# Optimization experiments

Hardware: AMD Instinct MI355X
Metric: run time of the kernel (lower is better)

## Reference

```python
import jax, jax.numpy as jnp
import numpy as np

EMBED_DIM = 1024
NUM_HEADS = 16
HEAD_DIM = EMBED_DIM // NUM_HEADS
SCALE = HEAD_DIM ** -0.5


def setup_inputs() -> dict:
    key = jax.random.key(0)
    ks = jax.random.split(key, 11)
    b, n, c = 2, 2048, EMBED_DIM
    # xavier_uniform bound for square [c, c] weight
    bound = float(np.sqrt(6.0 / (c + c)))
    def xavier(k):
        return jax.random.uniform(k, (c, c), jnp.float32, -bound, bound)
    return {
        "q": jax.random.normal(ks[0], (b, n, c), jnp.float32),
        "k": jax.random.normal(ks[1], (b, n, c), jnp.float32),
        "v": jax.random.normal(ks[2], (b, n, c), jnp.float32),
        "wq": xavier(ks[3]), "bq": jnp.zeros((c,), jnp.float32),
        "wk": xavier(ks[4]), "bk": jnp.zeros((c,), jnp.float32),
        "wv": xavier(ks[5]), "bv": jnp.zeros((c,), jnp.float32),
        "wo": xavier(ks[6]), "bo": jnp.zeros((c,), jnp.float32),
    }


def reference(q, k, v, wq, bq, wk, bk, wv, bv, wo, bo):
    b, n, c = q.shape
    h, d = NUM_HEADS, HEAD_DIM
    # linear projections (torch Linear: x @ W^T + b)
    qh = (q @ wq.T + bq).reshape(b, n, h, d).transpose(0, 2, 1, 3)  # b h n d
    kh = (k @ wk.T + bk).reshape(b, n, h, d).transpose(0, 2, 1, 3)
    vh = (v @ wv.T + bv).reshape(b, n, h, d).transpose(0, 2, 1, 3)
    dots = jnp.einsum('bhid,bhjd->bhij', qh, kh) * SCALE
    attn = jax.nn.softmax(dots, axis=-1)  # dropout p=0 -> identity
    out = jnp.einsum('bhij,bhjd->bhid', attn, vh)
    out = out.transpose(0, 2, 1, 3).reshape(b, n, c)
    return out @ wo.T + bo
```

## Files before the change

### kernel.cpp

```cpp
#include <hip/hip_runtime.h>


typedef float f32x4 __attribute__((ext_vector_type(4)));
typedef float f32x16 __attribute__((ext_vector_type(16)));
typedef __bf16 bf16x8 __attribute__((ext_vector_type(8)));

#define SEQ 2048
#define CH 1024
#define NH 16
#define HD 64
#define TOK 4096
#define QSCALE 0.18033688011112042f

__device__ __forceinline__ unsigned short f2b(float f) {
  unsigned int u = __float_as_uint(f);
  u = (u + 0x7FFFu + ((u >> 16) & 1u)) >> 16;
  return (unsigned short)u;
}

__device__ __forceinline__ unsigned int cvtpk(float lo, float hi) {
  unsigned int r;
  asm("v_cvt_pk_bf16_f32 %0, %1, %2" : "=v"(r) : "v"(lo), "v"(hi));
  return r;
}

__device__ __forceinline__ void gload16(const void* g, void* l) {
  __builtin_amdgcn_global_load_lds(
      (const __attribute__((address_space(1))) unsigned int*)g,
      (__attribute__((address_space(3))) unsigned int*)l, 16, 0, 0);
}

struct CvtArgs {
  const float* src[7];
  unsigned short* dst[7];
  int n4[7];
};

__global__ __launch_bounds__(256) void cvt_kernel(CvtArgs a) {
  const int s = blockIdx.y;
  const int n4 = a.n4[s];
  const float4* __restrict__ src = (const float4*)a.src[s];
  unsigned short* __restrict__ dst = a.dst[s];
  const int stride = gridDim.x * blockDim.x;
  for (int i = blockIdx.x * blockDim.x + threadIdx.x; i < n4; i += stride) {
    float4 w = src[i];
    ushort4 o;
    o.x = f2b(w.x); o.y = f2b(w.y); o.z = f2b(w.z); o.w = f2b(w.w);
    *(ushort4*)(dst + 4 * (size_t)i) = o;
  }
}

struct ProjArgs {
  const unsigned short* X[2];
  const unsigned short* W[2];
  const float* bias[2];
  unsigned short* outb[2];
  float* outf;
  int mode[2];
};

__device__ __forceinline__ void proj_stage(
    const unsigned short* __restrict__ X, const unsigned short* __restrict__ W,
    int mt, int nt, int k0, unsigned char* buf, int wid, int lane) {
#pragma unroll
  for (int is = 0; is < 2; ++is) {
    const int p = (wid * 2 + is) * 1024 + lane * 16;
    gload16(X + (size_t)(mt * 128 + (p >> 6)) * CH + k0 + ((p & 63) >> 1),
            buf + (wid * 2 + is) * 1024);
  }
  {
    const int p = wid * 1024 + lane * 16;
    gload16(W + (size_t)(nt * 64 + (p >> 6)) * CH + k0 + ((p & 63) >> 1),
            buf + 8192 + wid * 1024);
  }
}

__global__ __launch_bounds__(256, 4) void proj_kernel(ProjArgs a) {
  constexpr int BUFB = 8192 + 4096;
  __shared__ __align__(16) unsigned char smem[3 * BUFB];
  const int z = blockIdx.z;
  const unsigned short* __restrict__ X = a.X[z];
  const unsigned short* __restrict__ W = a.W[z];
  const float* __restrict__ bias = a.bias[z];
  unsigned short* __restrict__ outb = a.outb[z];
  float* __restrict__ outf = a.outf;
  const int mode = a.mode[z];
  const int tid = threadIdx.x, wid = tid >> 6, lane = tid & 63;
  const int wm = wid >> 1, wn = wid & 1;
  const int mt = blockIdx.x, nt = blockIdx.y;
  const int l15 = lane & 15, l4 = lane >> 4;

  float bvv[2];
#pragma unroll
  for (int nj = 0; nj < 2; ++nj)
    bvv[nj] = bias[nt * 64 + wn * 32 + nj * 16 + l15];

  f32x4 acc[4][2] = {};

  proj_stage(X, W, mt, nt, 0, smem, wid, lane);
  proj_stage(X, W, mt, nt, 32, smem + BUFB, wid, lane);

  for (int s = 0; s < 32; ++s) {
    if (s < 31) asm volatile("s_waitcnt vmcnt(3)" ::: "memory");
    else        asm volatile("s_waitcnt vmcnt(0)" ::: "memory");
    __builtin_amdgcn_s_barrier();
    __builtin_amdgcn_sched_barrier(0);
    if (s + 2 < 32)
      proj_stage(X, W, mt, nt, (s + 2) * 32, smem + ((s + 2) % 3) * BUFB, wid, lane);

    unsigned char* Al = smem + (s % 3) * BUFB;
    unsigned char* Bl = Al + 8192;
    bf16x8 af[4], bfr[2];
#pragma unroll
    for (int mi = 0; mi < 4; ++mi)
      af[mi] = *(const bf16x8*)(Al + (wm * 64 + mi * 16 + l15) * 64 + l4 * 16);
#pragma unroll
    for (int nj = 0; nj < 2; ++nj)
      bfr[nj] = *(const bf16x8*)(Bl + (wn * 32 + nj * 16 + l15) * 64 + l4 * 16);
    __builtin_amdgcn_s_setprio(1);
#pragma unroll
    for (int mi = 0; mi < 4; ++mi)
#pragma unroll
      for (int nj = 0; nj < 2; ++nj)
        acc[mi][nj] = __builtin_amdgcn_mfma_f32_16x16x32_bf16(af[mi], bfr[nj], acc[mi][nj], 0, 0, 0);
    __builtin_amdgcn_s_setprio(0);
  }

  const int row0 = mt * 128 + wm * 64;
  const int col0 = nt * 64 + wn * 32;
#pragma unroll
  for (int nj = 0; nj < 2; ++nj) {
    const int col = col0 + nj * 16 + l15;
    const float bv = bvv[nj];
    const int h = col >> 6, d = col & 63;
    if (mode == 3) {
#pragma unroll
      for (int mi = 0; mi < 4; ++mi) {
        const int row = row0 + mi * 16 + l4 * 4;
        const int b = row >> 11, n = row & (SEQ - 1);
        ushort4 o;
        o.x = f2b(acc[mi][nj][0] + bv);
        o.y = f2b(acc[mi][nj][1] + bv);
        o.z = f2b(acc[mi][nj][2] + bv);
        o.w = f2b(acc[mi][nj][3] + bv);
        *(ushort4*)(outb + ((size_t)(b * NH + h) * HD + d) * SEQ + n) = o;
      }
    } else {
#pragma unroll
      for (int mi = 0; mi < 4; ++mi) {
#pragma unroll
        for (int r = 0; r < 4; ++r) {
          const int row = row0 + mi * 16 + l4 * 4 + r;
          float v = acc[mi][nj][r] + bv;
          if (mode == 0) v *= QSCALE;
          if (mode == 2) {
            outf[(size_t)row * CH + col] = v;
          } else {
            const int b = row >> 11, n = row & (SEQ - 1);
            outb[(((size_t)(b * NH + h) * SEQ + n) << 6) + d] = f2b(v);
          }
        }
      }
    }
  }
}

__device__ __forceinline__ void stage_kv(
    const unsigned short* __restrict__ Kb, const unsigned short* __restrict__ Vb,
    int j0, unsigned char* buf, int wid, int lane) {
#pragma unroll
  for (int is = 0; is < 2; ++is) {
    const int p = wid * 2048 + is * 1024 + lane * 16;
    const int row = p >> 7;
    const int sw = ((p & 127) ^ ((row & 7) << 4)) >> 1;
    gload16(Kb + (size_t)(j0 + row) * HD + sw, buf + wid * 2048 + is * 1024);
    gload16(Vb + (size_t)row * SEQ + j0 + sw, buf + 8192 + wid * 2048 + is * 1024);
  }
}

__global__ __launch_bounds__(256, 2) void attn_kernel(
    const unsigned short* __restrict__ Qh, const unsigned short* __restrict__ Kh,
    const unsigned short* __restrict__ Vt, unsigned short* __restrict__ AO) {
  __shared__ __align__(16) unsigned char smem[49152];
  const int tid = threadIdx.x, wid = tid >> 6, lane = tid & 63;
  const int l31 = lane & 31, h = lane >> 5;
  const int bid = blockIdx.x;
  const int swz = (bid & 7) * 64 + (bid >> 3);
  const int qt = swz & 15, bh = swz >> 4;

  const unsigned short* Qb = Qh + ((size_t)bh * SEQ + qt * 128) * HD;
  const unsigned short* Kb = Kh + (size_t)bh * SEQ * HD;
  const unsigned short* Vb = Vt + (size_t)bh * HD * SEQ;

#pragma unroll
  for (int is = 0; is < 4; ++is) {
    const int p = wid * 4096 + is * 1024 + lane * 16;
    const int row = p >> 7;
    const int sw = ((p & 127) ^ ((row & 7) << 4)) >> 1;
    gload16(Qb + (size_t)row * HD + sw, smem + 32768 + wid * 4096 + is * 1024);
  }
  stage_kv(Kb, Vb, 0, smem, wid, lane);
  asm volatile("s_waitcnt vmcnt(4)" ::: "memory");

  bf16x8 qf[4];
  const int qrow = wid * 32 + l31;
#pragma unroll
  for (int ks = 0; ks < 4; ++ks)
    qf[ks] = *(const bf16x8*)(smem + 32768 + qrow * 128 +
                              ((ks * 32 + h * 16) ^ ((qrow & 7) << 4)));
  asm volatile("s_waitcnt lgkmcnt(0)" ::: "memory");

  stage_kv(Kb, Vb, 64, smem + 16384, wid, lane);

  f32x16 O[2] = {};
  float m = -1e30f, l = 0.f;

  for (int it = 0; it < 32; ++it) {
    if (it < 31) asm volatile("s_waitcnt vmcnt(4)" ::: "memory");
    else         asm volatile("s_waitcnt vmcnt(0)" ::: "memory");
    __builtin_amdgcn_s_barrier();
    __builtin_amdgcn_sched_barrier(0);
    if (it + 2 < 32)
      stage_kv(Kb, Vb, (it + 2) * 64, smem + ((it + 2) % 3) * 16384, wid, lane);

    unsigned char* Kc = smem + (it % 3) * 16384;
    unsigned char* Vc = Kc + 8192;

    f32x16 st[2] = {};
    __builtin_amdgcn_s_setprio(1);
#pragma unroll
    for (int kb = 0; kb < 2; ++kb) {
#pragma unroll
      for (int ks = 0; ks < 4; ++ks) {
        const int krow = kb * 32 + l31;
        const bf16x8 kf = *(const bf16x8*)(Kc + krow * 128 +
                                           ((ks * 32 + h * 16) ^ ((krow & 7) << 4)));
        st[kb] = __builtin_amdgcn_mfma_f32_32x32x16_bf16(kf, qf[ks], st[kb], 0, 0, 0);
      }
    }
    __builtin_amdgcn_s_setprio(0);

    float t[8];
#pragma unroll
    for (int i = 0; i < 8; ++i)
      t[i] = fmaxf(fmaxf(st[0][i], st[0][i + 8]), fmaxf(st[1][i], st[1][i + 8]));
#pragma unroll
    for (int i = 0; i < 4; ++i) t[i] = fmaxf(t[i], t[i + 4]);
    float pmax = fmaxf(fmaxf(t[0], t[1]), fmaxf(t[2], t[3]));
    pmax = fmaxf(pmax, __shfl_xor(pmax, 32));
    if (__any(pmax > m + 8.f)) {
      const float mnew = fmaxf(m, pmax);
      const float alpha = exp2f(m - mnew);
#pragma unroll
      for (int r = 0; r < 16; ++r) {
        const int qO = (r & 3) + 8 * (r >> 2) + 4 * h;
        const float aO = __shfl(alpha, qO);
        O[0][r] *= aO;
        O[1][r] *= aO;
      }
      l *= alpha;
      m = mnew;
    }
#pragma unroll
    for (int kb = 0; kb < 2; ++kb)
#pragma unroll
      for (int i = 0; i < 16; ++i) st[kb][i] = exp2f(st[kb][i] - m);
    float s[8];
#pragma unroll
    for (int i = 0; i < 8; ++i)
      s[i] = (st[0][i] + st[0][i + 8]) + (st[1][i] + st[1][i + 8]);
#pragma unroll
    for (int i = 0; i < 4; ++i) s[i] += s[i + 4];
    float rs = (s[0] + s[1]) + (s[2] + s[3]);
    rs += __shfl_xor(rs, 32);
    l += rs;

    unsigned int pk[2][8];
#pragma unroll
    for (int kb = 0; kb < 2; ++kb)
#pragma unroll
      for (int j = 0; j < 8; ++j)
        pk[kb][j] = cvtpk(st[kb][2 * j], st[kb][2 * j + 1]);

    __builtin_amdgcn_s_setprio(1);
#pragma unroll
    for (int kk = 0; kk < 4; ++kk) {
      const int kb = kk >> 1, j0 = (kk & 1) * 4;
      const unsigned int p0 = pk[kb][j0 + 0], p1 = pk[kb][j0 + 1];
      const unsigned int p2 = pk[kb][j0 + 2], p3 = pk[kb][j0 + 3];
      const unsigned int u0 = h ? p0 : p2;
      const unsigned int u1 = h ? p1 : p3;
      const unsigned int su0 = __shfl_xor(u0, 32);
      const unsigned int su1 = __shfl_xor(u1, 32);
      const unsigned int d0 = h ? su0 : p0;
      const unsigned int d1 = h ? su1 : p1;
      const unsigned int d2 = h ? p2 : su0;
      const unsigned int d3 = h ? p3 : su1;
      uint4 aw = make_uint4(d0, d1, d2, d3);
      const bf16x8 af = *(const bf16x8*)&aw;
#pragma unroll
      for (int db = 0; db < 2; ++db) {
        const int vrow = db * 32 + l31;
        const bf16x8 vf = *(const bf16x8*)(Vc + vrow * 128 +
                                           ((kk * 32 + h * 16) ^ ((vrow & 7) << 4)));
        O[db] = __builtin_amdgcn_mfma_f32_32x32x16_bf16(af, vf, O[db], 0, 0, 0);
      }
    }
    __builtin_amdgcn_s_setprio(0);
  }

  const int b = bh >> 4, hh = bh & 15;
#pragma unroll
  for (int r = 0; r < 16; ++r) {
    const int qO = (r & 3) + 8 * (r >> 2) + 4 * h;
    const float lO = __shfl(l, qO);
    const float inv = 1.f / lO;
    const int n = qt * 128 + wid * 32 + qO;
    const size_t base = ((size_t)(b * SEQ + n)) * CH + hh * HD;
    AO[base + l31] = f2b(O[0][r] * inv);
    AO[base + 32 + l31] = f2b(O[1][r] * inv);
  }
}

extern "C" void kernel_launch(void* const* d_in, const int* in_sizes, int n_in,
                              void* d_out, int out_size, void* d_ws, size_t ws_size,
                              hipStream_t stream) {
  (void)in_sizes; (void)n_in; (void)out_size; (void)ws_size;
  const float* q  = (const float*)d_in[0];
  const float* k  = (const float*)d_in[1];
  const float* v  = (const float*)d_in[2];
  const float* wq = (const float*)d_in[3];
  const float* bq = (const float*)d_in[4];
  const float* wk = (const float*)d_in[5];
  const float* bk = (const float*)d_in[6];
  const float* wv = (const float*)d_in[7];
  const float* bv = (const float*)d_in[8];
  const float* wo = (const float*)d_in[9];
  const float* bo = (const float*)d_in[10];

  unsigned char* ws = (unsigned char*)d_ws;
  const size_t MB8 = 8u << 20;
  unsigned short* qb  = (unsigned short*)(ws + 0 * MB8);
  unsigned short* kb  = (unsigned short*)(ws + 1 * MB8);
  unsigned short* vb  = (unsigned short*)(ws + 2 * MB8);
  unsigned short* wqb = (unsigned short*)(ws + 3 * MB8);
  unsigned short* wkb = (unsigned short*)(ws + 3 * MB8 + 1 * 2097152);
  unsigned short* wvb = (unsigned short*)(ws + 3 * MB8 + 2 * 2097152);
  unsigned short* wob = (unsigned short*)(ws + 3 * MB8 + 3 * 2097152);
  unsigned short* Qh  = (unsigned short*)(ws + 4 * MB8);
  unsigned short* Kh  = (unsigned short*)(ws + 5 * MB8);
  unsigned short* VtT = kb;
  unsigned short* AO  = qb;
  float* out = (float*)d_out;

  CvtArgs ca;
  ca.src[0] = q;  ca.dst[0] = qb;  ca.n4[0] = TOK * CH / 4;
  ca.src[1] = k;  ca.dst[1] = kb;  ca.n4[1] = TOK * CH / 4;
  ca.src[2] = v;  ca.dst[2] = vb;  ca.n4[2] = TOK * CH / 4;
  ca.src[3] = wq; ca.dst[3] = wqb; ca.n4[3] = CH * CH / 4;
  ca.src[4] = wk; ca.dst[4] = wkb; ca.n4[4] = CH * CH / 4;
  ca.src[5] = wv; ca.dst[5] = wvb; ca.n4[5] = CH * CH / 4;
  ca.src[6] = wo; ca.dst[6] = wob; ca.n4[6] = CH * CH / 4;
  cvt_kernel<<<dim3(1024, 7), 256, 0, stream>>>(ca);

  ProjArgs qk;
  qk.X[0] = qb;  qk.W[0] = wqb; qk.bias[0] = bq; qk.outb[0] = Qh; qk.mode[0] = 0;
  qk.X[1] = kb;  qk.W[1] = wkb; qk.bias[1] = bk; qk.outb[1] = Kh; qk.mode[1] = 1;
  qk.outf = nullptr;
  proj_kernel<<<dim3(32, 16, 2), 256, 0, stream>>>(qk);

  ProjArgs vp;
  vp.X[0] = vb;  vp.W[0] = wvb; vp.bias[0] = bv; vp.outb[0] = VtT; vp.mode[0] = 3;
  vp.X[1] = vb;  vp.W[1] = wvb; vp.bias[1] = bv; vp.outb[1] = VtT; vp.mode[1] = 3;
  vp.outf = nullptr;
  proj_kernel<<<dim3(32, 16, 1), 256, 0, stream>>>(vp);

  attn_kernel<<<dim3(512), 256, 0, stream>>>(Qh, Kh, VtT, AO);

  ProjArgs op;
  op.X[0] = AO; op.W[0] = wob; op.bias[0] = bo; op.outb[0] = nullptr; op.mode[0] = 2;
  op.X[1] = AO; op.W[1] = wob; op.bias[1] = bo; op.outb[1] = nullptr; op.mode[1] = 2;
  op.outf = out;
  proj_kernel<<<dim3(32, 16, 1), 256, 0, stream>>>(op);
}
```

Before: 149.6 us.

## Split attention KV range across two wave groups per block and merge partials

The attention block grows from 256 to 512 threads. Two groups of four waves each handle half of the key/value sequence for the same 128 query rows, and each group runs its own double-buffered KV pipeline instead of the former triple-buffered one. The partial O, m and l from the second group are merged through shared memory with a log-sum-exp rescale before the output is written. exp2f is also replaced with raw v_exp_f32 inline asm. This doubles the waves working on each block to raise occupancy and latency hiding, at the cost of larger LDS use, an extra barrier per iteration, and a merge epilogue.

```diff
diff --git a/kernel.cpp b/kernel.cpp
--- a/kernel.cpp
+++ b/kernel.cpp
@@ -16,6 +16,12 @@
   unsigned int u = __float_as_uint(f);
   u = (u + 0x7FFFu + ((u >> 16) & 1u)) >> 16;
   return (unsigned short)u;
+}
+
+__device__ __forceinline__ float fexp2(float x) {
+  float r;
+  asm("v_exp_f32 %0, %1" : "=v"(r) : "v"(x));
+  return r;
 }
 
 __device__ __forceinline__ unsigned int cvtpk(float lo, float hi) {
@@ -167,23 +173,24 @@
 
 __device__ __forceinline__ void stage_kv(
     const unsigned short* __restrict__ Kb, const unsigned short* __restrict__ Vb,
-    int j0, unsigned char* buf, int wid, int lane) {
+    int j0, unsigned char* buf, int ws3, int lane) {
 #pragma unroll
   for (int is = 0; is < 2; ++is) {
-    const int p = wid * 2048 + is * 1024 + lane * 16;
+    const int p = ws3 * 2048 + is * 1024 + lane * 16;
     const int row = p >> 7;
     const int sw = ((p & 127) ^ ((row & 7) << 4)) >> 1;
-    gload16(Kb + (size_t)(j0 + row) * HD + sw, buf + wid * 2048 + is * 1024);
-    gload16(Vb + (size_t)row * SEQ + j0 + sw, buf + 8192 + wid * 2048 + is * 1024);
-  }
-}
-
-__global__ __launch_bounds__(256, 2) void attn_kernel(
+    gload16(Kb + (size_t)(j0 + row) * HD + sw, buf + ws3 * 2048 + is * 1024);
+    gload16(Vb + (size_t)row * SEQ + j0 + sw, buf + 8192 + ws3 * 2048 + is * 1024);
+  }
+}
+
+__global__ __launch_bounds__(512, 4) void attn_kernel(
     const unsigned short* __restrict__ Qh, const unsigned short* __restrict__ Kh,
     const unsigned short* __restrict__ Vt, unsigned short* __restrict__ AO) {
-  __shared__ __align__(16) unsigned char smem[49152];
+  __shared__ __align__(16) unsigned char smem[81920];
   const int tid = threadIdx.x, wid = tid >> 6, lane = tid & 63;
   const int l31 = lane & 31, h = lane >> 5;
+  const int grp = wid >> 2, wq = wid & 3;
   const int bid = blockIdx.x;
   const int swz = (bid & 7) * 64 + (bid >> 3);
   const int qt = swz & 15, bh = swz >> 4;
@@ -191,39 +198,39 @@
   const unsigned short* Qb = Qh + ((size_t)bh * SEQ + qt * 128) * HD;
   const unsigned short* Kb = Kh + (size_t)bh * SEQ * HD;
   const unsigned short* Vb = Vt + (size_t)bh * HD * SEQ;
+  unsigned char* kvb = smem + grp * 32768;
+  unsigned char* Qreg = smem + 65536;
+  const int jbase = grp * 16;
 
 #pragma unroll
   for (int is = 0; is < 4; ++is) {
-    const int p = wid * 4096 + is * 1024 + lane * 16;
+    const int p = wq * 4096 + is * 1024 + lane * 16;
     const int row = p >> 7;
     const int sw = ((p & 127) ^ ((row & 7) << 4)) >> 1;
-    gload16(Qb + (size_t)row * HD + sw, smem + 32768 + wid * 4096 + is * 1024);
-  }
-  stage_kv(Kb, Vb, 0, smem, wid, lane);
+    gload16(Qb + (size_t)row * HD + sw, Qreg + wq * 4096 + is * 1024);
+  }
+  stage_kv(Kb, Vb, jbase * 64, kvb, wq, lane);
   asm volatile("s_waitcnt vmcnt(4)" ::: "memory");
 
   bf16x8 qf[4];
-  const int qrow = wid * 32 + l31;
+  const int qrow = wq * 32 + l31;
 #pragma unroll
   for (int ks = 0; ks < 4; ++ks)
-    qf[ks] = *(const bf16x8*)(smem + 32768 + qrow * 128 +
+    qf[ks] = *(const bf16x8*)(Qreg + qrow * 128 +
                               ((ks * 32 + h * 16) ^ ((qrow & 7) << 4)));
-  asm volatile("s_waitcnt lgkmcnt(0)" ::: "memory");
-
-  stage_kv(Kb, Vb, 64, smem + 16384, wid, lane);
+
+  stage_kv(Kb, Vb, (jbase + 1) * 64, kvb + 16384, wq, lane);
 
   f32x16 O[2] = {};
   float m = -1e30f, l = 0.f;
 
-  for (int it = 0; it < 32; ++it) {
-    if (it < 31) asm volatile("s_waitcnt vmcnt(4)" ::: "memory");
+  for (int it = 0; it < 16; ++it) {
+    if (it < 15) asm volatile("s_waitcnt vmcnt(4)" ::: "memory");
     else         asm volatile("s_waitcnt vmcnt(0)" ::: "memory");
     __builtin_amdgcn_s_barrier();
     __builtin_amdgcn_sched_barrier(0);
-    if (it + 2 < 32)
-      stage_kv(Kb, Vb, (it + 2) * 64, smem + ((it + 2) % 3) * 16384, wid, lane);
-
-    unsigned char* Kc = smem + (it % 3) * 16384;
+
+    unsigned char* Kc = kvb + ((it & 1) << 14);
     unsigned char* Vc = Kc + 8192;
 
     f32x16 st[2] = {};
@@ -250,7 +257,7 @@
     pmax = fmaxf(pmax, __shfl_xor(pmax, 32));
     if (__any(pmax > m + 8.f)) {
       const float mnew = fmaxf(m, pmax);
-      const float alpha = exp2f(m - mnew);
+      const float alpha = fexp2(m - mnew);
 #pragma unroll
       for (int r = 0; r < 16; ++r) {
         const int qO = (r & 3) + 8 * (r >> 2) + 4 * h;
@@ -264,7 +271,7 @@
 #pragma unroll
     for (int kb = 0; kb < 2; ++kb)
 #pragma unroll
-      for (int i = 0; i < 16; ++i) st[kb][i] = exp2f(st[kb][i] - m);
+      for (int i = 0; i < 16; ++i) st[kb][i] = fexp2(st[kb][i] - m);
     float s[8];
 #pragma unroll
     for (int i = 0; i < 8; ++i)
@@ -307,18 +314,40 @@
       }
     }
     __builtin_amdgcn_s_setprio(0);
-  }
-
-  const int b = bh >> 4, hh = bh & 15;
-#pragma unroll
-  for (int r = 0; r < 16; ++r) {
-    const int qO = (r & 3) + 8 * (r >> 2) + 4 * h;
-    const float lO = __shfl(l, qO);
-    const float inv = 1.f / lO;
-    const int n = qt * 128 + wid * 32 + qO;
-    const size_t base = ((size_t)(b * SEQ + n)) * CH + hh * HD;
-    AO[base + l31] = f2b(O[0][r] * inv);
-    AO[base + 32 + l31] = f2b(O[1][r] * inv);
+
+    __builtin_amdgcn_s_barrier();
+    if (it + 2 < 16)
+      stage_kv(Kb, Vb, (jbase + it + 2) * 64, Kc, wq, lane);
+  }
+
+  float2* slotO = (float2*)(smem + wq * 8960);
+  float2* slotML = (float2*)(smem + wq * 8960 + 8704);
+  if (grp == 1) {
+    float2* dst = slotO + lane * 17;
+#pragma unroll
+    for (int i = 0; i < 8; ++i) dst[i] = make_float2(O[0][2 * i], O[0][2 * i + 1]);
+#pragma unroll
+    for (int i = 0; i < 8; ++i) dst[8 + i] = make_float2(O[1][2 * i], O[1][2 * i + 1]);
+    if (h == 0) slotML[l31] = make_float2(m, l);
+  }
+  __builtin_amdgcn_s_barrier();
+  if (grp == 0) {
+    const float* src = (const float*)(slotO + lane * 17);
+    const float2 ml1 = slotML[l31];
+    const float mm = fmaxf(m, ml1.x);
+    const float a0 = fexp2(m - mm), a1 = fexp2(ml1.x - mm);
+    const float inv = 1.f / (a0 * l + a1 * ml1.y);
+    const float w0 = a0 * inv, w1 = a1 * inv;
+    const int b = bh >> 4, hh = bh & 15;
+#pragma unroll
+    for (int r = 0; r < 16; ++r) {
+      const int qO = (r & 3) + 8 * (r >> 2) + 4 * h;
+      const float s0 = __shfl(w0, qO), s1 = __shfl(w1, qO);
+      const int n = qt * 128 + wq * 32 + qO;
+      const size_t base = ((size_t)(b * SEQ + n)) * CH + hh * HD;
+      AO[base + l31] = f2b(O[0][r] * s0 + src[r] * s1);
+      AO[base + 32 + l31] = f2b(O[1][r] * s0 + src[16 + r] * s1);
+    }
   }
 }
 
@@ -375,7 +404,7 @@
   vp.outf = nullptr;
   proj_kernel<<<dim3(32, 16, 1), 256, 0, stream>>>(vp);
 
-  attn_kernel<<<dim3(512), 256, 0, stream>>>(Qh, Kh, VtT, AO);
+  attn_kernel<<<dim3(512), 512, 0, stream>>>(Qh, Kh, VtT, AO);
 
   ProjArgs op;
   op.X[0] = AO; op.W[0] = wob; op.bias[0] = bo; op.outb[0] = nullptr; op.mode[0] = 2;
```

Result: faster. 134.4 us (-10.2%).
